# Optimization experiments

Measured on AMD Instinct MI355X. Metric: run time of the kernel, lower is better.

The kernel has to match this reference:

```python
import jax, jax.numpy as jnp
import numpy as np

N = 50000      # nodes
E = 800000     # edges
D_IN = 128     # input feature dim
HID = 64       # out_channels (per-head dim; concat=False -> head mean)
HEADS = 2
NEG_SLOPE = 0.2


def gat_layer(x, src, dst, Ws, Wd, a_s, a_d, b):
    # PyG GATConv, add_self_loops=False, concat=False (mean over heads)
    n = x.shape[0]
    H, C = a_s.shape
    hs = (x @ Ws).reshape(n, H, C)          # source-side features [N,H,C]
    hd = (x @ Wd).reshape(n, H, C)          # dest-side features   [N,H,C]
    als = (hs * a_s).sum(-1)                # [N,H]
    ald = (hd * a_d).sum(-1)                # [N,H]
    e = jax.nn.leaky_relu(als[src] + ald[dst], NEG_SLOPE)   # [E,H]
    # segment softmax over edges grouped by destination node
    m = jax.ops.segment_max(e, dst, num_segments=n)
    m = jax.lax.stop_gradient(jnp.where(jnp.isfinite(m), m, 0.0))
    ex = jnp.exp(e - m[dst])
    den = jax.ops.segment_sum(ex, dst, num_segments=n)
    alpha = ex / (den[dst] + 1e-16)                          # [E,H]
    out = jax.ops.segment_sum(hs[src] * alpha[:, :, None], dst, num_segments=n)
    return out.mean(axis=1) + b             # [N,C]


def setup_inputs() -> dict:
    key = jax.random.key(0)
    ks = jax.random.split(key, 32)
    d = {}
    d["x"] = jax.random.normal(ks[0], (N, D_IN), jnp.float32)
    d["edge_index"] = jax.random.randint(ks[1], (2, E), 0, N, jnp.int32)
    dins = [D_IN, HID, HID]
    i = 2
    for l in range(1, 4):
        din = dins[l - 1]
        s = 1.0 / np.sqrt(din)
        d[f"Ws{l}"] = jax.random.normal(ks[i], (din, HEADS * HID), jnp.float32) * s; i += 1
        d[f"Wd{l}"] = jax.random.normal(ks[i], (din, HEADS * HID), jnp.float32) * s; i += 1
        d[f"as{l}"] = jax.random.normal(ks[i], (HEADS, HID), jnp.float32) * 0.1; i += 1
        d[f"ad{l}"] = jax.random.normal(ks[i], (HEADS, HID), jnp.float32) * 0.1; i += 1
        d[f"b{l}"] = jnp.zeros((HID,), jnp.float32)
        d[f"Wl{l}"] = jax.random.normal(ks[i], (din, HID), jnp.float32) * s; i += 1
        d[f"bl{l}"] = jnp.zeros((HID,), jnp.float32)
    return d


def reference(x, edge_index,
              Ws1, Wd1, as1, ad1, b1, Wl1, bl1,
              Ws2, Wd2, as2, ad2, b2, Wl2, bl2,
              Ws3, Wd3, as3, ad3, b3, Wl3, bl3):
    src, dst = edge_index[0], edge_index[1]
    h = jax.nn.relu(gat_layer(x, src, dst, Ws1, Wd1, as1, ad1, b1) + x @ Wl1 + bl1)
    h = jax.nn.relu(gat_layer(h, src, dst, Ws2, Wd2, as2, ad2, b2) + h @ Wl2 + bl2)
    h = jax.nn.relu(gat_layer(h, src, dst, Ws3, Wd3, as3, ad3, b3) + h @ Wl3 + bl3)
    return h
```

## Files before the change

kernel.cpp:

```cpp
#include <hip/hip_runtime.h>
#include <hip/hip_bf16.h>

#define NN 50000
#define NE 800000
#define SCAN_BS 1024
#define SCAN_NB ((NN + SCAN_BS - 1) / SCAN_BS)
#define EB ((NE + 255) / 256)

typedef __attribute__((ext_vector_type(8))) __bf16 bf16x8;
typedef __attribute__((ext_vector_type(4))) float float4v;

__device__ __forceinline__ unsigned pack_bf2(float lo, float hi) {
    union { __bf16 b; unsigned short u; } a, c;
    a.b = (__bf16)lo; c.b = (__bf16)hi;
    return (unsigned)a.u | ((unsigned)c.u << 16);
}
__device__ __forceinline__ float2 unpack_bf2(unsigned v) {
    union { unsigned short u; __bf16 b; } lo, hi;
    lo.u = (unsigned short)(v & 0xffff); hi.u = (unsigned short)(v >> 16);
    return make_float2((float)lo.b, (float)hi.b);
}


__device__ __forceinline__ void convert_w_part(const float* __restrict__ Ws,
                                               const float* __restrict__ Wd,
                                               const float* __restrict__ Wl,
                                               __bf16* __restrict__ Wt, int K, int i)
{
    if (i >= 320 * K) return;
    int c = i / K, k = i % K;
    float v;
    if (c < 128)      v = Ws[k * 128 + c];
    else if (c < 256) v = Wd[k * 128 + (c - 128)];
    else              v = Wl[k * 64 + (c - 256)];
    Wt[i] = (__bf16)v;
}

__global__ void __launch_bounds__(256)
prep_kernel(const int* __restrict__ ei, int* __restrict__ deg, int* __restrict__ rank,
            const float* __restrict__ Ws1, const float* __restrict__ Wd1,
            const float* __restrict__ Wl1, __bf16* __restrict__ Wt1,
            const float* __restrict__ Ws2, const float* __restrict__ Wd2,
            const float* __restrict__ Wl2, __bf16* __restrict__ Wt2,
            const float* __restrict__ Ws3, const float* __restrict__ Wd3,
            const float* __restrict__ Wl3, __bf16* __restrict__ Wt3)
{
    int bi = blockIdx.x;
    if (bi < EB) {
        int e = bi * 256 + threadIdx.x;
        if (e < NE) rank[e] = atomicAdd(&deg[ei[NE + e]], 1);
    } else if (bi < EB + 160) {
        convert_w_part(Ws1, Wd1, Wl1, Wt1, 128, (bi - EB) * 256 + threadIdx.x);
    } else if (bi < EB + 240) {
        convert_w_part(Ws2, Wd2, Wl2, Wt2, 64, (bi - EB - 160) * 256 + threadIdx.x);
    } else {
        convert_w_part(Ws3, Wd3, Wl3, Wt3, 64, (bi - EB - 240) * 256 + threadIdx.x);
    }
}


__global__ void __launch_bounds__(SCAN_BS)
scan1_kernel(const int* __restrict__ deg, int* __restrict__ exl, int* __restrict__ bsum)
{
    __shared__ int sh[SCAN_BS];
    int t = threadIdx.x;
    int i = blockIdx.x * SCAN_BS + t;
    int v = (i < NN) ? deg[i] : 0;
    sh[t] = v;
    __syncthreads();
    for (int off = 1; off < SCAN_BS; off <<= 1) {
        int u = (t >= off) ? sh[t - off] : 0;
        __syncthreads();
        sh[t] += u;
        __syncthreads();
    }
    if (i < NN) exl[i] = sh[t] - v;
    if (t == SCAN_BS - 1) bsum[blockIdx.x] = sh[t];
}

__global__ void __launch_bounds__(64)
scan2_kernel(const int* __restrict__ bsum, int* __restrict__ boff, int* __restrict__ row)
{
    int l = threadIdx.x;
    int v = (l < SCAN_NB) ? bsum[l] : 0;
    int own = v;
    for (int off = 1; off < 64; off <<= 1) {
        int u = __shfl_up(v, off);
        if (l >= off) v += u;
    }
    if (l < SCAN_NB) boff[l] = v - own;
    if (l == 63) row[NN] = v;
}

__global__ void __launch_bounds__(SCAN_BS)
scan3_kernel(const int* __restrict__ exl, const int* __restrict__ boff,
             int* __restrict__ row)
{
    int i = blockIdx.x * SCAN_BS + threadIdx.x;
    if (i >= NN) return;
    row[i] = exl[i] + boff[blockIdx.x];
}

__global__ void __launch_bounds__(256)
scatter_kernel(const int* __restrict__ ei, const int* __restrict__ rank,
               const int* __restrict__ row, int* __restrict__ csr_src)
{
    int e = blockIdx.x * 256 + threadIdx.x;
    if (e >= NE) return;
    int s = ei[e], d = ei[NE + e];
    int p = row[d] + rank[e];
    csr_src[p] = s;
}


__device__ __forceinline__ bf16x8 load_af(const __bf16* p) { return *(const bf16x8*)p; }
__device__ __forceinline__ bf16x8 load_af(const float* p) {
    float4 u = *(const float4*)p;
    float4 v = *(const float4*)(p + 4);
    bf16x8 r;
    r[0] = (__bf16)u.x; r[1] = (__bf16)u.y; r[2] = (__bf16)u.z; r[3] = (__bf16)u.w;
    r[4] = (__bf16)v.x; r[5] = (__bf16)v.y; r[6] = (__bf16)v.z; r[7] = (__bf16)v.w;
    return r;
}

template <int K, typename TIN>
__global__ void __launch_bounds__(256)
mfma_gemm(const TIN* __restrict__ xin, const __bf16* __restrict__ Wt,
          const float* __restrict__ a_s, const float* __restrict__ a_d,
          unsigned* __restrict__ hsb, float* __restrict__ lin,
          float* __restrict__ als, float* __restrict__ ald)
{
    __shared__ __align__(16) char ldsW[320 * 144];

    const int tid  = threadIdx.x;
    const int lane = tid & 63;
    const int wave = tid >> 6;
    const int l15 = lane & 15, quad = lane >> 4;
    const int nblk0 = blockIdx.x * 64;
    const int n0 = nblk0 + wave * 16;
    const int nA = min(n0 + l15, NN - 1);

    bf16x8 afr[K / 32];
#pragma unroll
    for (int ks = 0; ks < K / 32; ++ks)
        afr[ks] = load_af(xin + (size_t)nA * K + ks * 32 + quad * 8);

    float4v acc[20];
#pragma unroll
    for (int t = 0; t < 20; ++t) acc[t] = (float4v){0.f, 0.f, 0.f, 0.f};

#pragma unroll
    for (int h = 0; h < K / 64; ++h) {
        uint4 tmp[10];
#pragma unroll
        for (int i = 0; i < 10; ++i) {
            int idx = i * 256 + tid;
            int r = idx >> 3, c = idx & 7;
            tmp[i] = *(const uint4*)(Wt + (size_t)r * K + h * 64 + c * 8);
        }
        if (h) __syncthreads();
#pragma unroll
        for (int i = 0; i < 10; ++i) {
            int idx = i * 256 + tid;
            int r = idx >> 3, c = idx & 7;
            *(uint4*)&ldsW[r * 144 + c * 16] = tmp[i];
        }
        __syncthreads();

#pragma unroll
        for (int ksh = 0; ksh < 2; ++ksh) {
            int ks = h * 2 + ksh;
#pragma unroll
            for (int t = 0; t < 20; ++t) {
                bf16x8 bf = *(const bf16x8*)&ldsW[(t * 16 + l15) * 144 + (ksh * 4 + quad) * 16];
                acc[t] = __builtin_amdgcn_mfma_f32_16x16x32_bf16(afr[ks], bf, acc[t], 0, 0, 0);
            }
        }
    }

    float s0[4], s1[4], d0[4], d1[4];
#pragma unroll
    for (int r = 0; r < 4; ++r) { s0[r] = 0.f; s1[r] = 0.f; d0[r] = 0.f; d1[r] = 0.f; }
#pragma unroll
    for (int t = 0; t < 4; ++t) {
        float as0 = a_s[t * 16 + l15];
        float as1 = a_s[64 + t * 16 + l15];
        float ad0 = a_d[t * 16 + l15];
        float ad1 = a_d[64 + t * 16 + l15];
#pragma unroll
        for (int r = 0; r < 4; ++r) {
            s0[r] += acc[t][r] * as0;
            s1[r] += acc[t + 4][r] * as1;
            d0[r] += acc[t + 8][r] * ad0;
            d1[r] += acc[t + 12][r] * ad1;
        }
    }
#pragma unroll
    for (int m = 1; m < 16; m <<= 1) {
#pragma unroll
        for (int r = 0; r < 4; ++r) {
            s0[r] += __shfl_xor(s0[r], m);
            s1[r] += __shfl_xor(s1[r], m);
            d0[r] += __shfl_xor(d0[r], m);
            d1[r] += __shfl_xor(d1[r], m);
        }
    }

    __syncthreads();
    unsigned* hs_l  = (unsigned*)ldsW;
    float*    lin_l = (float*)(ldsW + 64 * 68 * 4);
    float*    al_l  = (float*)(ldsW + 2 * 64 * 68 * 4);

#pragma unroll
    for (int t = 0; t < 4; ++t) {
#pragma unroll
        for (int r = 0; r < 4; ++r) {
            int ln = wave * 16 + quad * 4 + r;
            hs_l[ln * 68 + t * 16 + l15] = pack_bf2(acc[t][r], acc[t + 4][r]);
            lin_l[ln * 68 + t * 16 + l15] = acc[t + 16][r];
        }
    }
    if (l15 == 0) {
#pragma unroll
        for (int r = 0; r < 4; ++r) {
            int ln = wave * 16 + quad * 4 + r;
            al_l[0 * 64 + ln] = s0[r];
            al_l[1 * 64 + ln] = s1[r];
            al_l[2 * 64 + ln] = d0[r];
            al_l[3 * 64 + ln] = d1[r];
        }
    }
    __syncthreads();

#pragma unroll
    for (int it = 0; it < 4; ++it) {
        int idx4 = it * 256 + tid;
        int ln = idx4 >> 4, c4 = idx4 & 15;
        int n = nblk0 + ln;
        if (n < NN) {
            *(uint4*)&hsb[(size_t)n * 64 + c4 * 4] =
                *(const uint4*)&hs_l[ln * 68 + c4 * 4];
            *(float4*)&lin[(size_t)n * 64 + c4 * 4] =
                *(const float4*)&lin_l[ln * 68 + c4 * 4];
        }
    }
    {
        int half = tid >> 7;
        int t2 = tid & 127;
        int ln = t2 >> 1, h = t2 & 1;
        int n = nblk0 + ln;
        if (n < NN) {
            float v = al_l[(half * 2 + h) * 64 + ln];
            if (half == 0) als[n * 2 + h] = v;
            else           ald[n * 2 + h] = v;
        }
    }
}


__device__ __forceinline__ float2 edge_w(const float* __restrict__ als, int s,
                                         float ad0, float ad1)
{
    float2 al = *(const float2*)&als[s * 2];
    float e0 = al.x + ad0; e0 = (e0 >= 0.f) ? e0 : 0.2f * e0;
    float e1 = al.y + ad1; e1 = (e1 >= 0.f) ? e1 : 0.2f * e1;
    return make_float2(__expf(e0), __expf(e1));
}

__device__ __forceinline__ void store_q(float* p, float v0, float v1, float v2, float v3) {
    *(float4*)p = make_float4(v0, v1, v2, v3);
}
__device__ __forceinline__ void store_q(__bf16* p, float v0, float v1, float v2, float v3) {
    *(uint2*)p = make_uint2(pack_bf2(v0, v1), pack_bf2(v2, v3));
}

template <typename TO>
__global__ void __launch_bounds__(256)
gat_aggregate(const int* __restrict__ row, const int* __restrict__ csr_src,
              const float* __restrict__ als, const float* __restrict__ ald,
              const unsigned* __restrict__ hsb, const float* __restrict__ lin,
              const float* __restrict__ b, const float* __restrict__ bl,
              TO* __restrict__ out)
{
    int w = (blockIdx.x * 256 + threadIdx.x) >> 6;
    int lane = threadIdx.x & 63;
    int q = lane >> 4;
    int l15 = lane & 15;
    if (w >= NN) return;
    int p0 = row[w], p1 = row[w + 1];
    float ad0 = ald[w * 2 + 0];
    float ad1 = ald[w * 2 + 1];

    float a0[4] = {0.f, 0.f, 0.f, 0.f};
    float a1[4] = {0.f, 0.f, 0.f, 0.f};
    float den0 = 0.f, den1 = 0.f;

    int p = p0 + q;
    for (; p + 12 < p1; p += 16) {
        int sA = csr_src[p];
        int sB = csr_src[p + 4];
        int sC = csr_src[p + 8];
        int sD = csr_src[p + 12];
        float2 eA = edge_w(als, sA, ad0, ad1);
        float2 eB = edge_w(als, sB, ad0, ad1);
        float2 eC = edge_w(als, sC, ad0, ad1);
        float2 eD = edge_w(als, sD, ad0, ad1);
        uint4 gA = *(const uint4*)&hsb[(size_t)sA * 64 + 4 * l15];
        uint4 gB = *(const uint4*)&hsb[(size_t)sB * 64 + 4 * l15];
        uint4 gC = *(const uint4*)&hsb[(size_t)sC * 64 + 4 * l15];
        uint4 gD = *(const uint4*)&hsb[(size_t)sD * 64 + 4 * l15];
        den0 += (eA.x + eB.x) + (eC.x + eD.x);
        den1 += (eA.y + eB.y) + (eC.y + eD.y);
        float2 h;
        h = unpack_bf2(gA.x); a0[0] += eA.x * h.x; a1[0] += eA.y * h.y;
        h = unpack_bf2(gA.y); a0[1] += eA.x * h.x; a1[1] += eA.y * h.y;
        h = unpack_bf2(gA.z); a0[2] += eA.x * h.x; a1[2] += eA.y * h.y;
        h = unpack_bf2(gA.w); a0[3] += eA.x * h.x; a1[3] += eA.y * h.y;
        h = unpack_bf2(gB.x); a0[0] += eB.x * h.x; a1[0] += eB.y * h.y;
        h = unpack_bf2(gB.y); a0[1] += eB.x * h.x; a1[1] += eB.y * h.y;
        h = unpack_bf2(gB.z); a0[2] += eB.x * h.x; a1[2] += eB.y * h.y;
        h = unpack_bf2(gB.w); a0[3] += eB.x * h.x; a1[3] += eB.y * h.y;
        h = unpack_bf2(gC.x); a0[0] += eC.x * h.x; a1[0] += eC.y * h.y;
        h = unpack_bf2(gC.y); a0[1] += eC.x * h.x; a1[1] += eC.y * h.y;
        h = unpack_bf2(gC.z); a0[2] += eC.x * h.x; a1[2] += eC.y * h.y;
        h = unpack_bf2(gC.w); a0[3] += eC.x * h.x; a1[3] += eC.y * h.y;
        h = unpack_bf2(gD.x); a0[0] += eD.x * h.x; a1[0] += eD.y * h.y;
        h = unpack_bf2(gD.y); a0[1] += eD.x * h.x; a1[1] += eD.y * h.y;
        h = unpack_bf2(gD.z); a0[2] += eD.x * h.x; a1[2] += eD.y * h.y;
        h = unpack_bf2(gD.w); a0[3] += eD.x * h.x; a1[3] += eD.y * h.y;
    }
    for (; p + 4 < p1; p += 8) {
        int sA = csr_src[p];
        int sB = csr_src[p + 4];
        float2 eA = edge_w(als, sA, ad0, ad1);
        float2 eB = edge_w(als, sB, ad0, ad1);
        uint4 gA = *(const uint4*)&hsb[(size_t)sA * 64 + 4 * l15];
        uint4 gB = *(const uint4*)&hsb[(size_t)sB * 64 + 4 * l15];
        den0 += eA.x + eB.x;
        den1 += eA.y + eB.y;
        float2 h;
        h = unpack_bf2(gA.x); a0[0] += eA.x * h.x; a1[0] += eA.y * h.y;
        h = unpack_bf2(gA.y); a0[1] += eA.x * h.x; a1[1] += eA.y * h.y;
        h = unpack_bf2(gA.z); a0[2] += eA.x * h.x; a1[2] += eA.y * h.y;
        h = unpack_bf2(gA.w); a0[3] += eA.x * h.x; a1[3] += eA.y * h.y;
        h = unpack_bf2(gB.x); a0[0] += eB.x * h.x; a1[0] += eB.y * h.y;
        h = unpack_bf2(gB.y); a0[1] += eB.x * h.x; a1[1] += eB.y * h.y;
        h = unpack_bf2(gB.z); a0[2] += eB.x * h.x; a1[2] += eB.y * h.y;
        h = unpack_bf2(gB.w); a0[3] += eB.x * h.x; a1[3] += eB.y * h.y;
    }
    for (; p < p1; p += 4) {
        int s = csr_src[p];
        float2 e = edge_w(als, s, ad0, ad1);
        uint4 g = *(const uint4*)&hsb[(size_t)s * 64 + 4 * l15];
        den0 += e.x; den1 += e.y;
        float2 h;
        h = unpack_bf2(g.x); a0[0] += e.x * h.x; a1[0] += e.y * h.y;
        h = unpack_bf2(g.y); a0[1] += e.x * h.x; a1[1] += e.y * h.y;
        h = unpack_bf2(g.z); a0[2] += e.x * h.x; a1[2] += e.y * h.y;
        h = unpack_bf2(g.w); a0[3] += e.x * h.x; a1[3] += e.y * h.y;
    }

#pragma unroll
    for (int i = 0; i < 4; ++i) {
        a0[i] += __shfl_xor(a0[i], 16); a0[i] += __shfl_xor(a0[i], 32);
        a1[i] += __shfl_xor(a1[i], 16); a1[i] += __shfl_xor(a1[i], 32);
    }
    den0 += __shfl_xor(den0, 16); den0 += __shfl_xor(den0, 32);
    den1 += __shfl_xor(den1, 16); den1 += __shfl_xor(den1, 32);

    if (q == 0) {
        int c0 = 4 * l15;
        float r0 = 1.f / (den0 + 1e-16f);
        float r1 = 1.f / (den1 + 1e-16f);
        float4 lv = *(const float4*)&lin[(size_t)w * 64 + c0];
        float v0 = 0.5f * (a0[0] * r0 + a1[0] * r1) + b[c0 + 0] + bl[c0 + 0] + lv.x;
        float v1 = 0.5f * (a0[1] * r0 + a1[1] * r1) + b[c0 + 1] + bl[c0 + 1] + lv.y;
        float v2 = 0.5f * (a0[2] * r0 + a1[2] * r1) + b[c0 + 2] + bl[c0 + 2] + lv.z;
        float v3 = 0.5f * (a0[3] * r0 + a1[3] * r1) + b[c0 + 3] + bl[c0 + 3] + lv.w;
        store_q(&out[(size_t)w * 64 + c0],
                fmaxf(v0, 0.f), fmaxf(v1, 0.f), fmaxf(v2, 0.f), fmaxf(v3, 0.f));
    }
}


extern "C" void kernel_launch(void* const* d_in, const int* in_sizes, int n_in,
                              void* d_out, int out_size, void* d_ws, size_t ws_size,
                              hipStream_t stream)
{
    const float* x  = (const float*)d_in[0];
    const int*   ei = (const int*)d_in[1];
    const float* Ws[3]; const float* Wd[3]; const float* As[3]; const float* Ad[3];
    const float* Bb[3]; const float* Wl[3]; const float* Bl[3];
    for (int l = 0; l < 3; ++l) {
        int base = 2 + 7 * l;
        Ws[l] = (const float*)d_in[base + 0];
        Wd[l] = (const float*)d_in[base + 1];
        As[l] = (const float*)d_in[base + 2];
        Ad[l] = (const float*)d_in[base + 3];
        Bb[l] = (const float*)d_in[base + 4];
        Wl[l] = (const float*)d_in[base + 5];
        Bl[l] = (const float*)d_in[base + 6];
    }

    float* ws = (float*)d_ws;
    unsigned* hsb = (unsigned*)ws;
    float* lin  = (float*)(hsb + (size_t)NN * 64);
    float* als  = lin + (size_t)NN * 64;
    float* ald  = als + (size_t)NN * 2;
    __bf16* hb  = (__bf16*)(ald + (size_t)NN * 2);
    __bf16* Wt1 = hb + (size_t)NN * 64;
    __bf16* Wt2 = Wt1 + 320 * 128;
    __bf16* Wt3 = Wt2 + 320 * 64;
    int* row     = (int*)(Wt3 + 320 * 64);
    int* deg     = row + (NN + 1);
    int* rank    = deg + NN;
    int* exl     = rank + NE;
    int* bsum    = exl + NN;
    int* boff    = bsum + SCAN_NB;
    int* csr_src = boff + SCAN_NB;

    const int WB  = (NN * 64 + 255) / 256;
    const int GB  = (NN + 63) / 64;

    hipMemsetAsync(deg, 0, sizeof(int) * NN, stream);
    prep_kernel<<<EB + 320, 256, 0, stream>>>(ei, deg, rank,
        Ws[0], Wd[0], Wl[0], Wt1,
        Ws[1], Wd[1], Wl[1], Wt2,
        Ws[2], Wd[2], Wl[2], Wt3);
    scan1_kernel<<<SCAN_NB, SCAN_BS, 0, stream>>>(deg, exl, bsum);
    scan2_kernel<<<1, 64, 0, stream>>>(bsum, boff, row);
    scan3_kernel<<<SCAN_NB, SCAN_BS, 0, stream>>>(exl, boff, row);
    scatter_kernel<<<EB, 256, 0, stream>>>(ei, rank, row, csr_src);

    for (int l = 0; l < 3; ++l) {
        if (l == 0) {
            mfma_gemm<128, float><<<GB, 256, 0, stream>>>(
                x, Wt1, As[0], Ad[0], hsb, lin, als, ald);
        } else {
            const __bf16* wt = (l == 1) ? Wt2 : Wt3;
            mfma_gemm<64, __bf16><<<GB, 256, 0, stream>>>(
                hb, wt, As[l], Ad[l], hsb, lin, als, ald);
        }
        if (l == 2) {
            gat_aggregate<float><<<WB, 256, 0, stream>>>(
                row, csr_src, als, ald, hsb, lin, Bb[l], Bl[l], (float*)d_out);
        } else {
            gat_aggregate<__bf16><<<WB, 256, 0, stream>>>(
                row, csr_src, als, ald, hsb, lin, Bb[l], Bl[l], hb);
        }
    }
}
```

Before: 343.0 us.

## Drop row-offset kernel and fuse CSR scatter into first-layer GEMM launch

Removes the scan3 kernel that materialised row offsets and instead computes them on the fly from the local exclusive scan plus the block offset. The edge scatter into CSR order is merged into the first GEMM launch as extra blocks, so the two independent pieces of work share one dispatch. The aggregate kernel also loads its lin and bias vectors up front as float4 instead of scalar loads in the epilogue. This saves two launches and one pass over the row array, at the cost of an extra boff lookup per node and mixing blocks with very different shared-memory and runtime profiles in one grid.

```diff
diff --git a/kernel.cpp b/kernel.cpp
--- a/kernel.cpp
+++ b/kernel.cpp
@@ -6,6 +6,7 @@
 #define SCAN_BS 1024
 #define SCAN_NB ((NN + SCAN_BS - 1) / SCAN_BS)
 #define EB ((NE + 255) / 256)
+#define GB ((NN + 63) / 64)
 
 typedef __attribute__((ext_vector_type(8))) __bf16 bf16x8;
 typedef __attribute__((ext_vector_type(4))) float float4v;
@@ -79,7 +80,7 @@
 }
 
 __global__ void __launch_bounds__(64)
-scan2_kernel(const int* __restrict__ bsum, int* __restrict__ boff, int* __restrict__ row)
+scan2_kernel(const int* __restrict__ bsum, int* __restrict__ boff)
 {
     int l = threadIdx.x;
     int v = (l < SCAN_NB) ? bsum[l] : 0;
@@ -89,27 +90,6 @@
         if (l >= off) v += u;
     }
     if (l < SCAN_NB) boff[l] = v - own;
-    if (l == 63) row[NN] = v;
-}
-
-__global__ void __launch_bounds__(SCAN_BS)
-scan3_kernel(const int* __restrict__ exl, const int* __restrict__ boff,
-             int* __restrict__ row)
-{
-    int i = blockIdx.x * SCAN_BS + threadIdx.x;
-    if (i >= NN) return;
-    row[i] = exl[i] + boff[blockIdx.x];
-}
-
-__global__ void __launch_bounds__(256)
-scatter_kernel(const int* __restrict__ ei, const int* __restrict__ rank,
-               const int* __restrict__ row, int* __restrict__ csr_src)
-{
-    int e = blockIdx.x * 256 + threadIdx.x;
-    if (e >= NE) return;
-    int s = ei[e], d = ei[NE + e];
-    int p = row[d] + rank[e];
-    csr_src[p] = s;
 }
 
 
@@ -124,19 +104,18 @@
 }
 
 template <int K, typename TIN>
-__global__ void __launch_bounds__(256)
-mfma_gemm(const TIN* __restrict__ xin, const __bf16* __restrict__ Wt,
-          const float* __restrict__ a_s, const float* __restrict__ a_d,
-          unsigned* __restrict__ hsb, float* __restrict__ lin,
-          float* __restrict__ als, float* __restrict__ ald)
-{
-    __shared__ __align__(16) char ldsW[320 * 144];
-
+__device__ __forceinline__ void gemm_body(
+    int bi, char* ldsW,
+    const TIN* __restrict__ xin, const __bf16* __restrict__ Wt,
+    const float* __restrict__ a_s, const float* __restrict__ a_d,
+    unsigned* __restrict__ hsb, float* __restrict__ lin,
+    float* __restrict__ als, float* __restrict__ ald)
+{
     const int tid  = threadIdx.x;
     const int lane = tid & 63;
     const int wave = tid >> 6;
     const int l15 = lane & 15, quad = lane >> 4;
-    const int nblk0 = blockIdx.x * 64;
+    const int nblk0 = bi * 64;
     const int n0 = nblk0 + wave * 16;
     const int nA = min(n0 + l15, NN - 1);
 
@@ -257,6 +236,39 @@
     }
 }
 
+__global__ void __launch_bounds__(256)
+gemm1_scatter_kernel(const float* __restrict__ x, const __bf16* __restrict__ Wt,
+                     const float* __restrict__ a_s, const float* __restrict__ a_d,
+                     unsigned* __restrict__ hsb, float* __restrict__ lin,
+                     float* __restrict__ als, float* __restrict__ ald,
+                     const int* __restrict__ ei, const int* __restrict__ rank,
+                     const int* __restrict__ exl, const int* __restrict__ boff,
+                     int* __restrict__ csr_src)
+{
+    __shared__ __align__(16) char ldsW[320 * 144];
+    if (blockIdx.x < GB) {
+        gemm_body<128, float>(blockIdx.x, ldsW, x, Wt, a_s, a_d, hsb, lin, als, ald);
+    } else {
+        int e = (blockIdx.x - GB) * 256 + threadIdx.x;
+        if (e < NE) {
+            int s = ei[e], d = ei[NE + e];
+            int p = exl[d] + boff[d >> 10] + rank[e];
+            csr_src[p] = s;
+        }
+    }
+}
+
+template <int K, typename TIN>
+__global__ void __launch_bounds__(256)
+mfma_gemm(const TIN* __restrict__ xin, const __bf16* __restrict__ Wt,
+          const float* __restrict__ a_s, const float* __restrict__ a_d,
+          unsigned* __restrict__ hsb, float* __restrict__ lin,
+          float* __restrict__ als, float* __restrict__ ald)
+{
+    __shared__ __align__(16) char ldsW[320 * 144];
+    gemm_body<K, TIN>(blockIdx.x, ldsW, xin, Wt, a_s, a_d, hsb, lin, als, ald);
+}
+
 
 __device__ __forceinline__ float2 edge_w(const float* __restrict__ als, int s,
                                          float ad0, float ad1)
@@ -276,7 +288,8 @@
 
 template <typename TO>
 __global__ void __launch_bounds__(256)
-gat_aggregate(const int* __restrict__ row, const int* __restrict__ csr_src,
+gat_aggregate(const int* __restrict__ exl, const int* __restrict__ boff,
+              const int* __restrict__ csr_src,
               const float* __restrict__ als, const float* __restrict__ ald,
               const unsigned* __restrict__ hsb, const float* __restrict__ lin,
               const float* __restrict__ b, const float* __restrict__ bl,
@@ -287,9 +300,15 @@
     int q = lane >> 4;
     int l15 = lane & 15;
     if (w >= NN) return;
-    int p0 = row[w], p1 = row[w + 1];
+    int p0 = exl[w] + boff[w >> 10];
+    int p1 = (w + 1 < NN) ? (exl[w + 1] + boff[(w + 1) >> 10]) : NE;
     float ad0 = ald[w * 2 + 0];
     float ad1 = ald[w * 2 + 1];
+
+    int c0 = 4 * l15;
+    float4 lv = *(const float4*)&lin[(size_t)w * 64 + c0];
+    float4 bv = *(const float4*)&b[c0];
+    float4 blv = *(const float4*)&bl[c0];
 
     float a0[4] = {0.f, 0.f, 0.f, 0.f};
     float a1[4] = {0.f, 0.f, 0.f, 0.f};
@@ -369,14 +388,12 @@
     den1 += __shfl_xor(den1, 16); den1 += __shfl_xor(den1, 32);
 
     if (q == 0) {
-        int c0 = 4 * l15;
         float r0 = 1.f / (den0 + 1e-16f);
         float r1 = 1.f / (den1 + 1e-16f);
-        float4 lv = *(const float4*)&lin[(size_t)w * 64 + c0];
-        float v0 = 0.5f * (a0[0] * r0 + a1[0] * r1) + b[c0 + 0] + bl[c0 + 0] + lv.x;
-        float v1 = 0.5f * (a0[1] * r0 + a1[1] * r1) + b[c0 + 1] + bl[c0 + 1] + lv.y;
-        float v2 = 0.5f * (a0[2] * r0 + a1[2] * r1) + b[c0 + 2] + bl[c0 + 2] + lv.z;
-        float v3 = 0.5f * (a0[3] * r0 + a1[3] * r1) + b[c0 + 3] + bl[c0 + 3] + lv.w;
+        float v0 = 0.5f * (a0[0] * r0 + a1[0] * r1) + bv.x + blv.x + lv.x;
+        float v1 = 0.5f * (a0[1] * r0 + a1[1] * r1) + bv.y + blv.y + lv.y;
+        float v2 = 0.5f * (a0[2] * r0 + a1[2] * r1) + bv.z + blv.z + lv.z;
+        float v3 = 0.5f * (a0[3] * r0 + a1[3] * r1) + bv.w + blv.w + lv.w;
         store_q(&out[(size_t)w * 64 + c0],
                 fmaxf(v0, 0.f), fmaxf(v1, 0.f), fmaxf(v2, 0.f), fmaxf(v3, 0.f));
     }
@@ -411,16 +428,14 @@
     __bf16* Wt1 = hb + (size_t)NN * 64;
     __bf16* Wt2 = Wt1 + 320 * 128;
     __bf16* Wt3 = Wt2 + 320 * 64;
-    int* row     = (int*)(Wt3 + 320 * 64);
-    int* deg     = row + (NN + 1);
+    int* deg     = (int*)(Wt3 + 320 * 64);
     int* rank    = deg + NN;
     int* exl     = rank + NE;
     int* bsum    = exl + NN;
     int* boff    = bsum + SCAN_NB;
     int* csr_src = boff + SCAN_NB;
 
-    const int WB  = (NN * 64 + 255) / 256;
-    const int GB  = (NN + 63) / 64;
+    const int WB = (NN * 64 + 255) / 256;
 
     hipMemsetAsync(deg, 0, sizeof(int) * NN, stream);
     prep_kernel<<<EB + 320, 256, 0, stream>>>(ei, deg, rank,
@@ -428,25 +443,23 @@
         Ws[1], Wd[1], Wl[1], Wt2,
         Ws[2], Wd[2], Wl[2], Wt3);
     scan1_kernel<<<SCAN_NB, SCAN_BS, 0, stream>>>(deg, exl, bsum);
-    scan2_kernel<<<1, 64, 0, stream>>>(bsum, boff, row);
-    scan3_kernel<<<SCAN_NB, SCAN_BS, 0, stream>>>(exl, boff, row);
-    scatter_kernel<<<EB, 256, 0, stream>>>(ei, rank, row, csr_src);
+    scan2_kernel<<<1, 64, 0, stream>>>(bsum, boff);
+
+    gemm1_scatter_kernel<<<GB + EB, 256, 0, stream>>>(
+        x, Wt1, As[0], Ad[0], hsb, lin, als, ald, ei, rank, exl, boff, csr_src);
 
     for (int l = 0; l < 3; ++l) {
-        if (l == 0) {
-            mfma_gemm<128, float><<<GB, 256, 0, stream>>>(
-                x, Wt1, As[0], Ad[0], hsb, lin, als, ald);
-        } else {
+        if (l > 0) {
             const __bf16* wt = (l == 1) ? Wt2 : Wt3;
             mfma_gemm<64, __bf16><<<GB, 256, 0, stream>>>(
                 hb, wt, As[l], Ad[l], hsb, lin, als, ald);
         }
         if (l == 2) {
             gat_aggregate<float><<<WB, 256, 0, stream>>>(
-                row, csr_src, als, ald, hsb, lin, Bb[l], Bl[l], (float*)d_out);
+                exl, boff, csr_src, als, ald, hsb, lin, Bb[l], Bl[l], (float*)d_out);
         } else {
             gat_aggregate<__bf16><<<WB, 256, 0, stream>>>(
-                row, csr_src, als, ald, hsb, lin, Bb[l], Bl[l], hb);
-        }
-    }
-}
+                exl, boff, csr_src, als, ald, hsb, lin, Bb[l], Bl[l], hb);
+        }
+    }
+}
```

New measurement: 360.1 us. 1.05x slower.
